# Kernel tuning notes

Hardware: AMD Instinct MI355X
Metric: run time of the kernel (lower is better)

The kernel has to match this reference:

```python
import math
import jax, jax.numpy as jnp
import numpy as np

ANCHORS_SETTINGS = (
    dict(layer='p3', stride=32, size=48, scale=[2 ** (1.0 / 3.0), 2 ** (2.0 / 3.0)], aspect_ratio=[0.667, 1, 1.5]),
    dict(layer='p4', stride=64, size=96, scale=[2 ** (1.0 / 3.0), 2 ** (2.0 / 3.0)], aspect_ratio=[0.667, 1, 1.5]),
    dict(layer='p5', stride=128, size=192, scale=[1, 2 ** (1.0 / 3.0), 2 ** (2.0 / 3.0)], aspect_ratio=[0.667, 1, 1.5]),
)


def anchor_configs():
    # 21 static (kernel, stride, padding) configs, in the exact counter order of
    # weighted_anchor_aggregator (p3 x6, p4 x6, p5 x9).
    cfgs = []
    for info in ANCHORS_SETTINGS:
        stride, size = info['stride'], info['size']
        for scale in info['scale']:
            for ar in info['aspect_ratio']:
                kernel = (int(size * scale / float(ar) ** 0.5), int(size * scale * float(ar) ** 0.5))
                padding = (math.ceil((kernel[0] - stride) / 2.0), math.ceil((kernel[1] - stride) / 2.0))
                cfgs.append((kernel, (stride, stride), padding))
    return cfgs


def extract_weighted_patches(x, weights, kernel, stride, padding):
    # x: (B,H,W,C); weights: (B,k,gh,gw). Vectorized equivalent of the original
    # lax.scan over per-position dynamic_slice gathers:
    #   acc = sum_{i,j} weights[:,:,i,j] (x) x_pad[:, i*s : i*s+kh, j*s : j*s+kw, :]
    b = x.shape[0]
    _, k, gh, gw = weights.shape
    xp = jnp.pad(x, ((0, 0),
                     (padding[0], padding[0] + kernel[0]),
                     (padding[1], padding[1] + kernel[1]),
                     (0, 0)))
    rows = jnp.arange(gh)[:, None] * stride[0] + jnp.arange(kernel[0])[None, :]  # (gh, kh)
    cols = jnp.arange(gw)[:, None] * stride[1] + jnp.arange(kernel[1])[None, :]  # (gw, kw)
    # gather all strided patches: (B, gh, kh, gw, kw, C)
    patches = xp[:, rows][:, :, :, cols]
    # weighted sum over grid positions -> (B, k, kh, kw, C)
    return jnp.einsum('bkij,bihjwc->bkhwc', weights, patches)


def _aggregate(x, weights_p3, weights_p4, weights_p5):
    weights = ([weights_p3[:, a] for a in range(weights_p3.shape[1])]
               + [weights_p4[:, a] for a in range(weights_p4.shape[1])]
               + [weights_p5[:, a] for a in range(weights_p5.shape[1])])
    b, k = weights[0].shape[0], weights[0].shape[1]
    acc = jnp.zeros((b * k, 224, 224, 3), x.dtype)
    for w, (kernel, stride, padding) in zip(weights, anchor_configs()):
        agg = extract_weighted_patches(x, w, kernel, stride, padding)
        agg = agg.reshape(b * k, kernel[0], kernel[1], 3)
        acc = acc + jax.image.resize(agg, (b * k, 224, 224, 3), 'bilinear')
    return acc


def setup_inputs() -> dict:
    key = jax.random.key(0)
    k0, k1, k2, k3 = jax.random.split(key, 4)
    B, K = 8, 4
    return {
        'x': jax.random.normal(k0, (B, 448, 448, 3), jnp.float32),
        'weights_p3': jax.random.uniform(k1, (B, 6, K, 14, 14), jnp.float32),
        'weights_p4': jax.random.uniform(k2, (B, 6, K, 7, 7), jnp.float32),
        'weights_p5': jax.random.uniform(k3, (B, 9, K, 4, 4), jnp.float32),
    }


def reference(x, weights_p3, weights_p4, weights_p5):
    return _aggregate(x, weights_p3, weights_p4, weights_p5)
```

## Files before the change

kernel.cpp:

```cpp
#include <hip/hip_runtime.h>
#include <math.h>


#define BATCH 8
#define KK 4
#define OUT_HW 224
#define IMG_HW 448
#define NCFG 21

#define WTBL_BYTES (NCFG * 2 * OUT_HW * 16)
#define ITBL_BYTES (NCFG * 2 * OUT_HW * 4)
#define WT_OFF_BYTES (WTBL_BYTES + ITBL_BYTES)
#define WT_F4 12912
#define AGG_OFF_BYTES (WT_OFF_BYTES + WT_F4 * 16)

#define REGION_PX 640

struct CfgEntry {
    int kh, kw;
    int mth, mtw;
    int tbl;
    int ws_off;
};

struct GroupArgs {
    CfgEntry e[NCFG];
    int n;
};

struct ACfg {
    int kh, kw, p0, p1;
    int layer;
    int qpr;
    int wt_off;
    int ws_off;
    int block_start;
    int blocks_per_img;
};

struct AggArgs {
    ACfg e[NCFG];
    int n;
};

struct TablesArgs { int kh[NCFG]; int kw[NCFG]; };

struct TrArgs {
    int layer[NCFG];
    int anchor[NCFG];
    int gsz[NCFG];
    int wt_off[NCFG];
};

struct F3 { float a, b, c; };
struct F6 { float f[6]; };

__device__ inline unsigned int bf16_rne(float f) {
    unsigned int u = __float_as_uint(f);
    return (u + 0x7fffu + ((u >> 16) & 1u)) >> 16;
}

__global__ __launch_bounds__(256) void init_tables(float4* __restrict__ wtbl,
                                                   int* __restrict__ itbl,
                                                   TablesArgs t) {
    int cfg = blockIdx.x >> 1;
    int dim = blockIdx.x & 1;
    int o = threadIdx.x;
    if (o >= OUT_HW) return;
    int n = dim ? t.kw[cfg] : t.kh[cfg];

    float inv = (float)(1.0 / ((double)OUT_HW / (double)n));
    float ks  = inv > 1.f ? inv : 1.f;
    float rks = 1.f / ks;
    float sf  = ((float)o + 0.5f) * inv - 0.5f;
    int i0 = (int)ceilf(sf - ks);  if (i0 < 0) i0 = 0;
    int i1 = (int)floorf(sf + ks); if (i1 > n - 1) i1 = n - 1;
    float sum = 0.f;
    for (int i = i0; i <= i1; ++i) {
        float v = 1.f - fabsf((float)i - sf) * rks;
        sum += (v > 0.f ? v : 0.f);
    }
    float rsum = 1.f / sum;
    float w[4];
#pragma unroll
    for (int d = 0; d < 4; ++d) {
        int i = i0 + d;
        float v = 0.f;
        if (i <= i1) {
            v = 1.f - fabsf((float)i - sf) * rks;
            v = (v > 0.f ? v : 0.f) * rsum;
        }
        w[d] = v;
    }
    int idx = cfg * (2 * OUT_HW) + dim * OUT_HW + o;
    wtbl[idx] = make_float4(w[0], w[1], w[2], w[3]);
    itbl[idx] = i0;
}

__global__ __launch_bounds__(256) void transpose_w(
        const float* __restrict__ wp3, const float* __restrict__ wp4,
        const float* __restrict__ wp5, float4* __restrict__ wT, TrArgs t) {
    int cfg = blockIdx.x;
    int b = blockIdx.y;
    int gsz = t.gsz[cfg];
    const float* base;
    int A;
    if (t.layer[cfg] == 0)      { base = wp3; A = 6; }
    else if (t.layer[cfg] == 1) { base = wp4; A = 6; }
    else                        { base = wp5; A = 9; }
    const float* src = base + (size_t)(b * A + t.anchor[cfg]) * (KK * gsz);
    for (int g = threadIdx.x; g < gsz; g += 256) {
        wT[t.wt_off[cfg] + b * gsz + g] =
            make_float4(src[0 * gsz + g], src[1 * gsz + g],
                        src[2 * gsz + g], src[3 * gsz + g]);
    }
}

template <int GH, int GW, int STRIDE>
__device__ inline void agg_body(const ACfg& c, int b, int h, int w0,
                                const float* __restrict__ xb,
                                const float4* __restrict__ wlds,
                                uint2* __restrict__ agg) {
    float acc[2][4][3] = {};

    const int rb = h - c.p0;
    int ilo = rb >= 0 ? 0 : (-rb + STRIDE - 1) / STRIDE;
    int ihi = (IMG_HW - 1 - rb) / STRIDE;
    if (ihi > GH - 1) ihi = GH - 1;

    const int cb = w0 - c.p1;

#pragma unroll 1
    for (int i = ilo; i <= ihi; ++i) {
        const float* xr = xb + (size_t)(rb + i * STRIDE) * (IMG_HW * 3);
        const float4* wrow = wlds + i * GW;
#pragma unroll
        for (int j = 0; j < GW; ++j) {
            int col = cb + j * STRIDE;
            float xv[6];
            bool any;
            if ((unsigned)col <= (unsigned)(IMG_HW - 2)) {
                F6 v = *(const F6*)(xr + (size_t)col * 3);
#pragma unroll
                for (int q = 0; q < 6; ++q) xv[q] = v.f[q];
                any = true;
            } else {
                bool ok0 = (unsigned)col < (unsigned)IMG_HW;
                bool ok1 = (unsigned)(col + 1) < (unsigned)IMG_HW;
                any = ok0 || ok1;
#pragma unroll
                for (int q = 0; q < 6; ++q) xv[q] = 0.f;
                if (ok0) {
                    F3 v = *(const F3*)(xr + (size_t)col * 3);
                    xv[0] = v.a; xv[1] = v.b; xv[2] = v.c;
                }
                if (ok1) {
                    F3 v = *(const F3*)(xr + (size_t)(col + 1) * 3);
                    xv[3] = v.a; xv[4] = v.b; xv[5] = v.c;
                }
            }
            if (any) {
                float4 wk = wrow[j];
#pragma unroll
                for (int t = 0; t < 2; ++t) {
                    float x0 = xv[t * 3 + 0], x1 = xv[t * 3 + 1], x2 = xv[t * 3 + 2];
                    acc[t][0][0] = fmaf(wk.x, x0, acc[t][0][0]);
                    acc[t][0][1] = fmaf(wk.x, x1, acc[t][0][1]);
                    acc[t][0][2] = fmaf(wk.x, x2, acc[t][0][2]);
                    acc[t][1][0] = fmaf(wk.y, x0, acc[t][1][0]);
                    acc[t][1][1] = fmaf(wk.y, x1, acc[t][1][1]);
                    acc[t][1][2] = fmaf(wk.y, x2, acc[t][1][2]);
                    acc[t][2][0] = fmaf(wk.z, x0, acc[t][2][0]);
                    acc[t][2][1] = fmaf(wk.z, x1, acc[t][2][1]);
                    acc[t][2][2] = fmaf(wk.z, x2, acc[t][2][2]);
                    acc[t][3][0] = fmaf(wk.w, x0, acc[t][3][0]);
                    acc[t][3][1] = fmaf(wk.w, x1, acc[t][3][1]);
                    acc[t][3][2] = fmaf(wk.w, x2, acc[t][3][2]);
                }
            }
        }
    }

    const int npix = c.kh * c.kw;
    const bool two = (w0 + 1) < c.kw;
#pragma unroll
    for (int k = 0; k < 4; ++k) {
        size_t base = (size_t)c.ws_off + (size_t)(b * KK + k) * npix
                    + (size_t)h * c.kw + w0;
        uint2 o0;
        o0.x = bf16_rne(acc[0][k][0]) | (bf16_rne(acc[0][k][1]) << 16);
        o0.y = bf16_rne(acc[0][k][2]);
        agg[base] = o0;
        if (two) {
            uint2 o1;
            o1.x = bf16_rne(acc[1][k][0]) | (bf16_rne(acc[1][k][1]) << 16);
            o1.y = bf16_rne(acc[1][k][2]);
            agg[base + 1] = o1;
        }
    }
}

__global__ __launch_bounds__(256, 4) void agg_all(
        const float* __restrict__ x,
        const float4* __restrict__ wT,
        uint2* __restrict__ agg,
        AggArgs a) {
    int bid = blockIdx.x;
    int ci = 0;
    while (ci + 1 < a.n && bid >= a.e[ci + 1].block_start) ci++;
    const ACfg c = a.e[ci];
    int local = bid - c.block_start;
    int b     = local / c.blocks_per_img;
    int sblk  = local - b * c.blocks_per_img;

    const int gsz = (c.layer == 0) ? 196 : (c.layer == 1) ? 49 : 16;
    __shared__ float4 wlds[196];
    for (int t = threadIdx.x; t < gsz; t += 256)
        wlds[t] = wT[c.wt_off + b * gsz + t];
    __syncthreads();

    int pidx = sblk * 256 + (int)threadIdx.x;
    if (pidx >= c.kh * c.qpr) return;
    int h  = pidx / c.qpr;
    int w0 = (pidx - h * c.qpr) * 2;

    const float* __restrict__ xb = x + (size_t)b * (IMG_HW * IMG_HW * 3);
    if (c.layer == 0)      agg_body<14, 14, 32>(c, b, h, w0, xb, wlds, agg);
    else if (c.layer == 1) agg_body<7, 7, 64>(c, b, h, w0, xb, wlds, agg);
    else                   agg_body<4, 4, 128>(c, b, h, w0, xb, wlds, agg);
}

template <int TH, int TW>
__device__ inline void taps(const uint2* __restrict__ rp0, int rcols,
                            float4 wh4, float4 ww4,
                            float& a0, float& a1, float& a2) {
    const float* wh = (const float*)&wh4;
    const float* ww = (const float*)&ww4;
#pragma unroll
    for (int d = 0; d < TH; ++d) {
        const uint2* rp = rp0 + d * rcols;
        float r0 = 0.f, r1 = 0.f, r2 = 0.f;
#pragma unroll
        for (int e = 0; e < TW; ++e) {
            uint2 v = rp[e];
            float c0 = __uint_as_float(v.x << 16);
            float c1 = __uint_as_float(v.x & 0xffff0000u);
            float c2 = __uint_as_float(v.y << 16);
            float w = ww[e];
            r0 = fmaf(w, c0, r0);
            r1 = fmaf(w, c1, r1);
            r2 = fmaf(w, c2, r2);
        }
        a0 = fmaf(wh[d], r0, a0);
        a1 = fmaf(wh[d], r1, a1);
        a2 = fmaf(wh[d], r2, a2);
    }
}

struct Win { int ri0, ci0, rrows, rcols; };

__global__ __launch_bounds__(256) void resize_kernel(
        const uint2* __restrict__ agg,
        const float4* __restrict__ wtbl,
        const int* __restrict__ itbl,
        float* __restrict__ out,
        GroupArgs g, int accumulate) {
    const int tid = threadIdx.x;
    const int tx = tid & 15;
    const int ty = tid >> 4;
    const int xo = blockIdx.x * 16 + tx;
    const int yo = blockIdx.y * 16 + ty;
    const int bk0 = blockIdx.z * 2;

    __shared__ float4 wlds[NCFG * 32];
    __shared__ int    ilds[NCFG * 32];
    __shared__ uint2  region[2 * REGION_PX];

    const int nent = g.n * 32;
    for (int e = tid; e < nent; e += 256) {
        int ci  = e >> 5;
        int r   = e & 31;
        int isW = r >> 4;
        int idx = r & 15;
        int base_o = isW ? (blockIdx.x * 16) : (blockIdx.y * 16);
        int src = g.e[ci].tbl * (2 * OUT_HW) + isW * OUT_HW + base_o + idx;
        wlds[ci * 32 + r] = wtbl[src];
        ilds[ci * 32 + r] = itbl[src];
    }
    __syncthreads();

    const int scc = tid & 31;
    const int srw = tid >> 5;

    uint2 sreg[2][4];
    Win wn, wc;

    {
        const CfgEntry c0 = g.e[0];
        int ri0 = ilds[0 * 32 + 0];
        int ri1 = ilds[0 * 32 + 15] + c0.mth - 1;
        int ci0 = ilds[0 * 32 + 16];
        int ci1 = ilds[0 * 32 + 31] + c0.mtw - 1;
        wn.ri0 = ri0; wn.ci0 = ci0;
        wn.rrows = ri1 - ri0 + 1; wn.rcols = ci1 - ci0 + 1;
        const int npx = c0.kh * c0.kw;
        const uint2* base = agg + (size_t)c0.ws_off + (size_t)bk0 * npx;
        int gj = ci0 + scc; if (gj > c0.kw - 1) gj = c0.kw - 1;
        bool cok = scc < wn.rcols;
#pragma unroll
        for (int s = 0; s < 4; ++s) {
            int r = srw + s * 8;
            if (cok && r < wn.rrows) {
                int gi = ri0 + r; if (gi > c0.kh - 1) gi = c0.kh - 1;
                size_t o = (size_t)gi * c0.kw + gj;
                sreg[0][s] = base[o];
                sreg[1][s] = base[o + npx];
            }
        }
    }

    size_t ob0 = (((size_t)bk0 * OUT_HW + yo) * OUT_HW + xo) * 3;
    size_t ob1 = ob0 + (size_t)OUT_HW * OUT_HW * 3;
    float a0, a1, a2, b0, b1, b2;
    if (accumulate) {
        a0 = out[ob0]; a1 = out[ob0 + 1]; a2 = out[ob0 + 2];
        b0 = out[ob1]; b1 = out[ob1 + 1]; b2 = out[ob1 + 2];
    } else {
        a0 = a1 = a2 = b0 = b1 = b2 = 0.f;
    }

    for (int c = 0; c < g.n; ++c) {
        wc = wn;
        __syncthreads();
        {
            bool cok = scc < wc.rcols;
#pragma unroll
            for (int s = 0; s < 4; ++s) {
                int r = srw + s * 8;
                if (cok && r < wc.rrows) {
                    int o = r * wc.rcols + scc;
                    region[o] = sreg[0][s];
                    region[REGION_PX + o] = sreg[1][s];
                }
            }
        }
        __syncthreads();

        if (c + 1 < g.n) {
            const CfgEntry cn = g.e[c + 1];
            int ri0 = ilds[(c + 1) * 32 + 0];
            int ri1 = ilds[(c + 1) * 32 + 15] + cn.mth - 1;
            int ci0 = ilds[(c + 1) * 32 + 16];
            int ci1 = ilds[(c + 1) * 32 + 31] + cn.mtw - 1;
            wn.ri0 = ri0; wn.ci0 = ci0;
            wn.rrows = ri1 - ri0 + 1; wn.rcols = ci1 - ci0 + 1;
            const int npx = cn.kh * cn.kw;
            const uint2* base = agg + (size_t)cn.ws_off + (size_t)bk0 * npx;
            int gj = ci0 + scc; if (gj > cn.kw - 1) gj = cn.kw - 1;
            bool cok = scc < wn.rcols;
#pragma unroll
            for (int s = 0; s < 4; ++s) {
                int r = srw + s * 8;
                if (cok && r < wn.rrows) {
                    int gi = ri0 + r; if (gi > cn.kh - 1) gi = cn.kh - 1;
                    size_t o = (size_t)gi * cn.kw + gj;
                    sreg[0][s] = base[o];
                    sreg[1][s] = base[o + npx];
                }
            }
        }

        float4 wh4 = wlds[c * 32 + ty];
        float4 ww4 = wlds[c * 32 + 16 + tx];
        int i0 = ilds[c * 32 + ty];
        int j0 = ilds[c * 32 + 16 + tx];
        int roff = (i0 - wc.ri0) * wc.rcols + (j0 - wc.ci0);
        const uint2* rp0 = region + roff;
        const uint2* rp1 = region + REGION_PX + roff;

        switch ((g.e[c].mth << 2) | g.e[c].mtw) {
            case (2 << 2) | 2:
                taps<2, 2>(rp0, wc.rcols, wh4, ww4, a0, a1, a2);
                taps<2, 2>(rp1, wc.rcols, wh4, ww4, b0, b1, b2); break;
            case (3 << 2) | 2:
                taps<3, 2>(rp0, wc.rcols, wh4, ww4, a0, a1, a2);
                taps<3, 2>(rp1, wc.rcols, wh4, ww4, b0, b1, b2); break;
            case (2 << 2) | 3:
                taps<2, 3>(rp0, wc.rcols, wh4, ww4, a0, a1, a2);
                taps<2, 3>(rp1, wc.rcols, wh4, ww4, b0, b1, b2); break;
            case (3 << 2) | 3:
                taps<3, 3>(rp0, wc.rcols, wh4, ww4, a0, a1, a2);
                taps<3, 3>(rp1, wc.rcols, wh4, ww4, b0, b1, b2); break;
            case (4 << 2) | 3:
                taps<4, 3>(rp0, wc.rcols, wh4, ww4, a0, a1, a2);
                taps<4, 3>(rp1, wc.rcols, wh4, ww4, b0, b1, b2); break;
            case (3 << 2) | 4:
                taps<3, 4>(rp0, wc.rcols, wh4, ww4, a0, a1, a2);
                taps<3, 4>(rp1, wc.rcols, wh4, ww4, b0, b1, b2); break;
            default:
                taps<4, 4>(rp0, wc.rcols, wh4, ww4, a0, a1, a2);
                taps<4, 4>(rp1, wc.rcols, wh4, ww4, b0, b1, b2); break;
        }
    }

    out[ob0 + 0] = a0; out[ob0 + 1] = a1; out[ob0 + 2] = a2;
    out[ob1 + 0] = b0; out[ob1 + 1] = b1; out[ob1 + 2] = b2;
}

extern "C" void kernel_launch(void* const* d_in, const int* in_sizes, int n_in,
                              void* d_out, int out_size, void* d_ws, size_t ws_size,
                              hipStream_t stream) {
    const float* x   = (const float*)d_in[0];
    const float* wp3 = (const float*)d_in[1];
    const float* wp4 = (const float*)d_in[2];
    const float* wp5 = (const float*)d_in[3];
    float* out = (float*)d_out;
    float4* wtbl = (float4*)d_ws;
    int*    itbl = (int*)((char*)d_ws + WTBL_BYTES);
    float4* wT   = (float4*)((char*)d_ws + WT_OFF_BYTES);
    uint2*  agg  = (uint2*)((char*)d_ws + AGG_OFF_BYTES);

    struct { int stride, size, nscale; double scales[3]; int gh; } layers[3] = {
        {32, 48, 2, {pow(2.0, 1.0 / 3.0), pow(2.0, 2.0 / 3.0), 0.0}, 14},
        {64, 96, 2, {pow(2.0, 1.0 / 3.0), pow(2.0, 2.0 / 3.0), 0.0}, 7},
        {128, 192, 3, {1.0, pow(2.0, 1.0 / 3.0), pow(2.0, 2.0 / 3.0)}, 4},
    };
    const double ars[3] = {0.667, 1.0, 1.5};

    struct HostCfg {
        int kh, kw, stride, p0, p1, gh, gw, layer, anchor, mth, mtw, wt_off;
        int qpr, blocks_per_img;
    } cfg[NCFG];
    TablesArgs ta;
    TrArgs tr;
    int nc = 0, wt_run = 0;
    for (int L = 0; L < 3; ++L) {
        int anchor = 0;
        for (int si = 0; si < layers[L].nscale; ++si) {
            for (int ai = 0; ai < 3; ++ai) {
                double ss = (double)layers[L].size * layers[L].scales[si];
                double sq = pow(ars[ai], 0.5);
                int kh = (int)(ss / sq);
                int kw = (int)(ss * sq);
                HostCfg& e = cfg[nc];
                e.kh = kh; e.kw = kw;
                e.stride = layers[L].stride;
                e.p0 = (int)ceil((double)(kh - layers[L].stride) / 2.0);
                e.p1 = (int)ceil((double)(kw - layers[L].stride) / 2.0);
                e.gh = layers[L].gh; e.gw = layers[L].gh;
                e.layer = L; e.anchor = anchor++;
                e.mth = (kh < OUT_HW) ? 2 : (int)((2.0 * kh) / OUT_HW) + 1;
                e.mtw = (kw < OUT_HW) ? 2 : (int)((2.0 * kw) / OUT_HW) + 1;
                if (e.mth > 4) e.mth = 4;
                if (e.mtw > 4) e.mtw = 4;
                e.qpr = (kw + 1) / 2;
                e.blocks_per_img = (kh * e.qpr + 255) / 256;
                e.wt_off = wt_run;
                int gsz = e.gh * e.gw;
                wt_run += BATCH * gsz;
                ta.kh[nc] = kh; ta.kw[nc] = kw;
                tr.layer[nc] = L; tr.anchor[nc] = e.anchor;
                tr.gsz[nc] = gsz; tr.wt_off[nc] = e.wt_off;
                ++nc;
            }
        }
    }

    init_tables<<<NCFG * 2, 256, 0, stream>>>(wtbl, itbl, ta);
    transpose_w<<<dim3(NCFG, BATCH), 256, 0, stream>>>(wp3, wp4, wp5, wT, tr);

    size_t cap_px = (ws_size - AGG_OFF_BYTES) / 8;
    dim3 rgrid(OUT_HW / 16, OUT_HW / 16, BATCH * KK / 2);

    int i = 0;
    int first = 1;
    while (i < NCFG) {
        int gstart = i;
        size_t used = 0;
        while (i < NCFG) {
            size_t need = (size_t)cfg[i].kh * cfg[i].kw * (BATCH * KK);
            if (i > gstart && used + need > cap_px) break;
            used += need;
            ++i;
            if (used >= cap_px) break;
        }
        GroupArgs g; g.n = 0;
        AggArgs aa; aa.n = 0;
        int ablocks = 0;
        size_t off = 0;
        for (int c = gstart; c < i; ++c) {
            ACfg& lc = aa.e[aa.n++];
            lc.kh = cfg[c].kh; lc.kw = cfg[c].kw;
            lc.p0 = cfg[c].p0; lc.p1 = cfg[c].p1;
            lc.layer = cfg[c].layer;
            lc.qpr = cfg[c].qpr;
            lc.wt_off = cfg[c].wt_off;
            lc.ws_off = (int)off;
            lc.block_start = ablocks;
            lc.blocks_per_img = cfg[c].blocks_per_img;
            ablocks += cfg[c].blocks_per_img * BATCH;
            CfgEntry& re = g.e[g.n++];
            re.kh = cfg[c].kh; re.kw = cfg[c].kw;
            re.mth = cfg[c].mth; re.mtw = cfg[c].mtw;
            re.tbl = c; re.ws_off = (int)off;
            off += (size_t)cfg[c].kh * cfg[c].kw * (BATCH * KK);
        }
        agg_all<<<ablocks, 256, 0, stream>>>(x, wT, agg, aa);
        resize_kernel<<<rgrid, 256, 0, stream>>>(agg, wtbl, itbl, out, g, first ? 0 : 1);
        first = 0;
    }
    (void)in_sizes; (void)n_in; (void)out_size;
}
```

Before: 327.2 us.

## Drop LDS region staging in resize and use branchless clamped loads in aggregation

```diff
diff --git a/kernel.cpp b/kernel.cpp
--- a/kernel.cpp
+++ b/kernel.cpp
@@ -13,8 +13,6 @@
 #define WT_OFF_BYTES (WTBL_BYTES + ITBL_BYTES)
 #define WT_F4 12912
 #define AGG_OFF_BYTES (WT_OFF_BYTES + WT_F4 * 16)
-
-#define REGION_PX 640
 
 struct CfgEntry {
     int kh, kw;
@@ -53,7 +51,6 @@
 };
 
 struct F3 { float a, b, c; };
-struct F6 { float f[6]; };
 
 __device__ inline unsigned int bf16_rne(float f) {
     unsigned int u = __float_as_uint(f);
@@ -137,47 +134,47 @@
 #pragma unroll
         for (int j = 0; j < GW; ++j) {
             int col = cb + j * STRIDE;
-            float xv[6];
-            bool any;
-            if ((unsigned)col <= (unsigned)(IMG_HW - 2)) {
-                F6 v = *(const F6*)(xr + (size_t)col * 3);
-#pragma unroll
-                for (int q = 0; q < 6; ++q) xv[q] = v.f[q];
-                any = true;
-            } else {
-                bool ok0 = (unsigned)col < (unsigned)IMG_HW;
-                bool ok1 = (unsigned)(col + 1) < (unsigned)IMG_HW;
-                any = ok0 || ok1;
-#pragma unroll
-                for (int q = 0; q < 6; ++q) xv[q] = 0.f;
-                if (ok0) {
-                    F3 v = *(const F3*)(xr + (size_t)col * 3);
-                    xv[0] = v.a; xv[1] = v.b; xv[2] = v.c;
-                }
-                if (ok1) {
-                    F3 v = *(const F3*)(xr + (size_t)(col + 1) * 3);
-                    xv[3] = v.a; xv[4] = v.b; xv[5] = v.c;
-                }
-            }
-            if (any) {
-                float4 wk = wrow[j];
-#pragma unroll
-                for (int t = 0; t < 2; ++t) {
-                    float x0 = xv[t * 3 + 0], x1 = xv[t * 3 + 1], x2 = xv[t * 3 + 2];
-                    acc[t][0][0] = fmaf(wk.x, x0, acc[t][0][0]);
-                    acc[t][0][1] = fmaf(wk.x, x1, acc[t][0][1]);
-                    acc[t][0][2] = fmaf(wk.x, x2, acc[t][0][2]);
-                    acc[t][1][0] = fmaf(wk.y, x0, acc[t][1][0]);
-                    acc[t][1][1] = fmaf(wk.y, x1, acc[t][1][1]);
-                    acc[t][1][2] = fmaf(wk.y, x2, acc[t][1][2]);
-                    acc[t][2][0] = fmaf(wk.z, x0, acc[t][2][0]);
-                    acc[t][2][1] = fmaf(wk.z, x1, acc[t][2][1]);
-                    acc[t][2][2] = fmaf(wk.z, x2, acc[t][2][2]);
-                    acc[t][3][0] = fmaf(wk.w, x0, acc[t][3][0]);
-                    acc[t][3][1] = fmaf(wk.w, x1, acc[t][3][1]);
-                    acc[t][3][2] = fmaf(wk.w, x2, acc[t][3][2]);
-                }
-            }
+            int cc0 = col;
+            if (cc0 < 0) cc0 = 0;
+            if (cc0 > IMG_HW - 1) cc0 = IMG_HW - 1;
+            int cc1 = col + 1;
+            if (cc1 < 0) cc1 = 0;
+            if (cc1 > IMG_HW - 1) cc1 = IMG_HW - 1;
+            F3 v0 = *(const F3*)(xr + (size_t)cc0 * 3);
+            F3 v1 = *(const F3*)(xr + (size_t)cc1 * 3);
+            bool k0 = (unsigned)col < (unsigned)IMG_HW;
+            bool k1 = (unsigned)(col + 1) < (unsigned)IMG_HW;
+            float x0 = k0 ? v0.a : 0.f;
+            float x1 = k0 ? v0.b : 0.f;
+            float x2 = k0 ? v0.c : 0.f;
+            float y0 = k1 ? v1.a : 0.f;
+            float y1 = k1 ? v1.b : 0.f;
+            float y2 = k1 ? v1.c : 0.f;
+            float4 wk = wrow[j];
+            acc[0][0][0] = fmaf(wk.x, x0, acc[0][0][0]);
+            acc[0][0][1] = fmaf(wk.x, x1, acc[0][0][1]);
+            acc[0][0][2] = fmaf(wk.x, x2, acc[0][0][2]);
+            acc[0][1][0] = fmaf(wk.y, x0, acc[0][1][0]);
+            acc[0][1][1] = fmaf(wk.y, x1, acc[0][1][1]);
+            acc[0][1][2] = fmaf(wk.y, x2, acc[0][1][2]);
+            acc[0][2][0] = fmaf(wk.z, x0, acc[0][2][0]);
+            acc[0][2][1] = fmaf(wk.z, x1, acc[0][2][1]);
+            acc[0][2][2] = fmaf(wk.z, x2, acc[0][2][2]);
+            acc[0][3][0] = fmaf(wk.w, x0, acc[0][3][0]);
+            acc[0][3][1] = fmaf(wk.w, x1, acc[0][3][1]);
+            acc[0][3][2] = fmaf(wk.w, x2, acc[0][3][2]);
+            acc[1][0][0] = fmaf(wk.x, y0, acc[1][0][0]);
+            acc[1][0][1] = fmaf(wk.x, y1, acc[1][0][1]);
+            acc[1][0][2] = fmaf(wk.x, y2, acc[1][0][2]);
+            acc[1][1][0] = fmaf(wk.y, y0, acc[1][1][0]);
+            acc[1][1][1] = fmaf(wk.y, y1, acc[1][1][1]);
+            acc[1][1][2] = fmaf(wk.y, y2, acc[1][1][2]);
+            acc[1][2][0] = fmaf(wk.z, y0, acc[1][2][0]);
+            acc[1][2][1] = fmaf(wk.z, y1, acc[1][2][1]);
+            acc[1][2][2] = fmaf(wk.z, y2, acc[1][2][2]);
+            acc[1][3][0] = fmaf(wk.w, y0, acc[1][3][0]);
+            acc[1][3][1] = fmaf(wk.w, y1, acc[1][3][1]);
+            acc[1][3][2] = fmaf(wk.w, y2, acc[1][3][2]);
         }
     }
 
@@ -231,21 +228,34 @@
 }
 
 template <int TH, int TW>
-__device__ inline void taps(const uint2* __restrict__ rp0, int rcols,
-                            float4 wh4, float4 ww4,
-                            float& a0, float& a1, float& a2) {
+__device__ inline void taps_direct(const uint2* __restrict__ base,
+                                   int kh, int kw, int i0, int j0,
+                                   float4 wh4, float4 ww4,
+                                   float& a0, float& a1, float& a2) {
     const float* wh = (const float*)&wh4;
     const float* ww = (const float*)&ww4;
+    uint2 v[TH][TW];
 #pragma unroll
     for (int d = 0; d < TH; ++d) {
-        const uint2* rp = rp0 + d * rcols;
+        int gi = i0 + d;
+        if (gi > kh - 1) gi = kh - 1;
+        const uint2* rp = base + (size_t)gi * kw;
+#pragma unroll
+        for (int e = 0; e < TW; ++e) {
+            int gj = j0 + e;
+            if (gj > kw - 1) gj = kw - 1;
+            v[d][e] = rp[gj];
+        }
+    }
+#pragma unroll
+    for (int d = 0; d < TH; ++d) {
         float r0 = 0.f, r1 = 0.f, r2 = 0.f;
 #pragma unroll
         for (int e = 0; e < TW; ++e) {
-            uint2 v = rp[e];
-            float c0 = __uint_as_float(v.x << 16);
-            float c1 = __uint_as_float(v.x & 0xffff0000u);
-            float c2 = __uint_as_float(v.y << 16);
+            uint2 t = v[d][e];
+            float c0 = __uint_as_float(t.x << 16);
+            float c1 = __uint_as_float(t.x & 0xffff0000u);
+            float c2 = __uint_as_float(t.y << 16);
             float w = ww[e];
             r0 = fmaf(w, c0, r0);
             r1 = fmaf(w, c1, r1);
@@ -256,8 +266,6 @@
         a2 = fmaf(wh[d], r2, a2);
     }
 }
-
-struct Win { int ri0, ci0, rrows, rcols; };
 
 __global__ __launch_bounds__(256) void resize_kernel(
         const uint2* __restrict__ agg,
@@ -270,11 +278,10 @@
     const int ty = tid >> 4;
     const int xo = blockIdx.x * 16 + tx;
     const int yo = blockIdx.y * 16 + ty;
-    const int bk0 = blockIdx.z * 2;
+    const int bk = blockIdx.z;
 
     __shared__ float4 wlds[NCFG * 32];
     __shared__ int    ilds[NCFG * 32];
-    __shared__ uint2  region[2 * REGION_PX];
 
     const int nent = g.n * 32;
     for (int e = tid; e < nent; e += 256) {
@@ -289,122 +296,49 @@
     }
     __syncthreads();
 
-    const int scc = tid & 31;
-    const int srw = tid >> 5;
-
-    uint2 sreg[2][4];
-    Win wn, wc;
-
-    {
-        const CfgEntry c0 = g.e[0];
-        int ri0 = ilds[0 * 32 + 0];
-        int ri1 = ilds[0 * 32 + 15] + c0.mth - 1;
-        int ci0 = ilds[0 * 32 + 16];
-        int ci1 = ilds[0 * 32 + 31] + c0.mtw - 1;
-        wn.ri0 = ri0; wn.ci0 = ci0;
-        wn.rrows = ri1 - ri0 + 1; wn.rcols = ci1 - ci0 + 1;
-        const int npx = c0.kh * c0.kw;
-        const uint2* base = agg + (size_t)c0.ws_off + (size_t)bk0 * npx;
-        int gj = ci0 + scc; if (gj > c0.kw - 1) gj = c0.kw - 1;
-        bool cok = scc < wn.rcols;
-#pragma unroll
-        for (int s = 0; s < 4; ++s) {
-            int r = srw + s * 8;
-            if (cok && r < wn.rrows) {
-                int gi = ri0 + r; if (gi > c0.kh - 1) gi = c0.kh - 1;
-                size_t o = (size_t)gi * c0.kw + gj;
-                sreg[0][s] = base[o];
-                sreg[1][s] = base[o + npx];
-            }
-        }
-    }
-
-    size_t ob0 = (((size_t)bk0 * OUT_HW + yo) * OUT_HW + xo) * 3;
-    size_t ob1 = ob0 + (size_t)OUT_HW * OUT_HW * 3;
-    float a0, a1, a2, b0, b1, b2;
+    size_t ob = (((size_t)bk * OUT_HW + yo) * OUT_HW + xo) * 3;
+    float a0, a1, a2;
     if (accumulate) {
-        a0 = out[ob0]; a1 = out[ob0 + 1]; a2 = out[ob0 + 2];
-        b0 = out[ob1]; b1 = out[ob1 + 1]; b2 = out[ob1 + 2];
+        a0 = out[ob]; a1 = out[ob + 1]; a2 = out[ob + 2];
     } else {
-        a0 = a1 = a2 = b0 = b1 = b2 = 0.f;
+        a0 = a1 = a2 = 0.f;
     }
 
     for (int c = 0; c < g.n; ++c) {
-        wc = wn;
-        __syncthreads();
-        {
-            bool cok = scc < wc.rcols;
-#pragma unroll
-            for (int s = 0; s < 4; ++s) {
-                int r = srw + s * 8;
-                if (cok && r < wc.rrows) {
-                    int o = r * wc.rcols + scc;
-                    region[o] = sreg[0][s];
-                    region[REGION_PX + o] = sreg[1][s];
-                }
-            }
-        }
-        __syncthreads();
-
-        if (c + 1 < g.n) {
-            const CfgEntry cn = g.e[c + 1];
-            int ri0 = ilds[(c + 1) * 32 + 0];
-            int ri1 = ilds[(c + 1) * 32 + 15] + cn.mth - 1;
-            int ci0 = ilds[(c + 1) * 32 + 16];
-            int ci1 = ilds[(c + 1) * 32 + 31] + cn.mtw - 1;
-            wn.ri0 = ri0; wn.ci0 = ci0;
-            wn.rrows = ri1 - ri0 + 1; wn.rcols = ci1 - ci0 + 1;
-            const int npx = cn.kh * cn.kw;
-            const uint2* base = agg + (size_t)cn.ws_off + (size_t)bk0 * npx;
-            int gj = ci0 + scc; if (gj > cn.kw - 1) gj = cn.kw - 1;
-            bool cok = scc < wn.rcols;
-#pragma unroll
-            for (int s = 0; s < 4; ++s) {
-                int r = srw + s * 8;
-                if (cok && r < wn.rrows) {
-                    int gi = ri0 + r; if (gi > cn.kh - 1) gi = cn.kh - 1;
-                    size_t o = (size_t)gi * cn.kw + gj;
-                    sreg[0][s] = base[o];
-                    sreg[1][s] = base[o + npx];
-                }
-            }
-        }
-
+        const CfgEntry e = g.e[c];
         float4 wh4 = wlds[c * 32 + ty];
         float4 ww4 = wlds[c * 32 + 16 + tx];
         int i0 = ilds[c * 32 + ty];
         int j0 = ilds[c * 32 + 16 + tx];
-        int roff = (i0 - wc.ri0) * wc.rcols + (j0 - wc.ci0);
-        const uint2* rp0 = region + roff;
-        const uint2* rp1 = region + REGION_PX + roff;
-
-        switch ((g.e[c].mth << 2) | g.e[c].mtw) {
+        const uint2* base = agg + (size_t)e.ws_off
+                          + (size_t)bk * ((size_t)e.kh * e.kw);
+
+        switch ((e.mth << 2) | e.mtw) {
             case (2 << 2) | 2:
-                taps<2, 2>(rp0, wc.rcols, wh4, ww4, a0, a1, a2);
-                taps<2, 2>(rp1, wc.rcols, wh4, ww4, b0, b1, b2); break;
+                taps_direct<2, 2>(base, e.kh, e.kw, i0, j0, wh4, ww4, a0, a1, a2);
+                break;
             case (3 << 2) | 2:
-                taps<3, 2>(rp0, wc.rcols, wh4, ww4, a0, a1, a2);
-                taps<3, 2>(rp1, wc.rcols, wh4, ww4, b0, b1, b2); break;
+                taps_direct<3, 2>(base, e.kh, e.kw, i0, j0, wh4, ww4, a0, a1, a2);
+                break;
             case (2 << 2) | 3:
-                taps<2, 3>(rp0, wc.rcols, wh4, ww4, a0, a1, a2);
-                taps<2, 3>(rp1, wc.rcols, wh4, ww4, b0, b1, b2); break;
+                taps_direct<2, 3>(base, e.kh, e.kw, i0, j0, wh4, ww4, a0, a1, a2);
+                break;
             case (3 << 2) | 3:
-                taps<3, 3>(rp0, wc.rcols, wh4, ww4, a0, a1, a2);
-                taps<3, 3>(rp1, wc.rcols, wh4, ww4, b0, b1, b2); break;
+                taps_direct<3, 3>(base, e.kh, e.kw, i0, j0, wh4, ww4, a0, a1, a2);
+                break;
             case (4 << 2) | 3:
-                taps<4, 3>(rp0, wc.rcols, wh4, ww4, a0, a1, a2);
-                taps<4, 3>(rp1, wc.rcols, wh4, ww4, b0, b1, b2); break;
+                taps_direct<4, 3>(base, e.kh, e.kw, i0, j0, wh4, ww4, a0, a1, a2);
+                break;
             case (3 << 2) | 4:
-                taps<3, 4>(rp0, wc.rcols, wh4, ww4, a0, a1, a2);
-                taps<3, 4>(rp1, wc.rcols, wh4, ww4, b0, b1, b2); break;
+                taps_direct<3, 4>(base, e.kh, e.kw, i0, j0, wh4, ww4, a0, a1, a2);
+                break;
             default:
-                taps<4, 4>(rp0, wc.rcols, wh4, ww4, a0, a1, a2);
-                taps<4, 4>(rp1, wc.rcols, wh4, ww4, b0, b1, b2); break;
-        }
-    }
-
-    out[ob0 + 0] = a0; out[ob0 + 1] = a1; out[ob0 + 2] = a2;
-    out[ob1 + 0] = b0; out[ob1 + 1] = b1; out[ob1 + 2] = b2;
+                taps_direct<4, 4>(base, e.kh, e.kw, i0, j0, wh4, ww4, a0, a1, a2);
+                break;
+        }
+    }
+
+    out[ob + 0] = a0; out[ob + 1] = a1; out[ob + 2] = a2;
 }
 
 extern "C" void kernel_launch(void* const* d_in, const int* in_sizes, int n_in,
@@ -470,7 +404,7 @@
     transpose_w<<<dim3(NCFG, BATCH), 256, 0, stream>>>(wp3, wp4, wp5, wT, tr);
 
     size_t cap_px = (ws_size - AGG_OFF_BYTES) / 8;
-    dim3 rgrid(OUT_HW / 16, OUT_HW / 16, BATCH * KK / 2);
+    dim3 rgrid(OUT_HW / 16, OUT_HW / 16, BATCH * KK);
 
     int i = 0;
     int first = 1;
```

Measured after the change: 306.4 us. 1.07x faster.
